# Optimization experiments

Measured on AMD Instinct MI355X. Metric: run time of the kernel, lower is better.

## Reference

```python
import jax, jax.numpy as jnp
import numpy as np
import math

B, S, V, E, H, MD, P, W = 2, 2048, 32000, 512, 1024, 256, 4096, 128

def setup_inputs() -> dict:
    key = jax.random.key(0)
    ks = jax.random.split(key, 24)
    sc = 0.02
    inp = {}
    inp['input_ids'] = jax.random.randint(ks[0], (B, S), 0, V)
    inp['untied_token_ids'] = jax.random.randint(ks[1], (P,), 0, V)
    inp['emb'] = jax.random.normal(ks[2], (V, E), jnp.float32) * sc
    inp['w_ih'] = jax.random.normal(ks[3], (3 * H, E), jnp.float32) * sc
    inp['w_hh'] = jax.random.normal(ks[4], (3 * H, H), jnp.float32) * sc
    inp['b_ih'] = jnp.zeros((3 * H,), jnp.float32)
    inp['b_hh'] = jnp.zeros((3 * H,), jnp.float32)
    inp['wq'] = jax.random.normal(ks[5], (MD, H), jnp.float32) * sc
    inp['bq'] = jnp.zeros((MD,), jnp.float32)
    inp['wk'] = jax.random.normal(ks[6], (MD, H), jnp.float32) * sc
    inp['bk'] = jnp.zeros((MD,), jnp.float32)
    inp['wv'] = jax.random.normal(ks[7], (E, H), jnp.float32) * sc
    inp['bv'] = jnp.zeros((E,), jnp.float32)
    inp['wg'] = jax.random.normal(ks[8], (1, H), jnp.float32) * sc
    inp['bg'] = jnp.zeros((1,), jnp.float32)
    inp['w_fc'] = jax.random.normal(ks[9], (4 * E, H), jnp.float32) * sc
    inp['b_fc'] = jnp.zeros((4 * E,), jnp.float32)
    inp['w_hp'] = jax.random.normal(ks[10], (E, 4 * E), jnp.float32) * sc
    inp['b_hp'] = jnp.zeros((E,), jnp.float32)
    inp['out_bias'] = jnp.zeros((V,), jnp.float32)
    inp['w_ph'] = jax.random.normal(ks[11], (P, E), jnp.float32) * sc
    inp['b_ph'] = jnp.zeros((P,), jnp.float32)
    inp['mem_scale'] = jnp.asarray(6.0, jnp.float32)
    return inp

def _gru(x, w_ih, w_hh, b_ih, b_hh):
    # x: [B,S,E] -> states [B,S,H]. Precompute input gates outside scan.
    gi = jnp.einsum('bse,ge->bsg', x, w_ih) + b_ih  # [B,S,3H]
    h0 = jnp.zeros((x.shape[0], w_hh.shape[1]), x.dtype)
    def step(h, gi_t):
        hg = h @ w_hh.T + b_hh
        gir, giz, gin = jnp.split(gi_t, 3, axis=-1)
        hgr, hgz, hgn = jnp.split(hg, 3, axis=-1)
        r = jax.nn.sigmoid(gir + hgr)
        z = jax.nn.sigmoid(giz + hgz)
        n = jnp.tanh(gin + r * hgn)
        h_new = (1.0 - z) * n + z * h
        return h_new, h_new
    _, hs = jax.lax.scan(step, h0, jnp.swapaxes(gi, 0, 1))  # [S,B,H]
    return jnp.swapaxes(hs, 0, 1)

def _forward(input_ids, untied_token_ids, emb, w_ih, w_hh, b_ih, b_hh, wq, bq,
             wk, bk, wv, bv, wg, bg, w_fc, b_fc, w_hp, b_hp, out_bias, w_ph,
             b_ph, mem_scale):
    x = emb[input_ids]                                   # [B,S,E]
    states = _gru(x, w_ih, w_hh, b_ih, b_hh)             # [B,S,H]
    hf = jnp.square(jax.nn.relu(states @ w_fc.T + b_fc)) # [B,S,4E]
    base_feat = hf @ w_hp.T + b_hp                       # [B,S,E]
    base_logits = base_feat @ emb.T + out_bias           # [B,S,V]
    base_partial = base_feat @ w_ph.T + b_ph             # [B,S,P]
    q = states @ wq.T + bq                               # [B,S,MD]
    k = states @ wk.T + bk
    v = states @ wv.T + bv                               # [B,S,E]
    scores = jnp.einsum('bqd,bkd->bqk', q, k) / math.sqrt(q.shape[-1])
    pos = jnp.arange(input_ids.shape[1])
    mask = (pos[None, :] < pos[:, None]) & (pos[None, :] >= pos[:, None] - W)
    neg = jnp.finfo(scores.dtype).min
    attn = jax.nn.softmax(jnp.where(mask[None], scores, neg), axis=-1)
    attn = attn * mask[None]
    attn = attn / jnp.clip(attn.sum(-1, keepdims=True), 1e-6)
    ctx = jnp.einsum('bqk,bke->bqe', attn, v)            # [B,S,E]
    gate = jax.nn.sigmoid(states @ wg.T + bg)            # [B,S,1]
    total_partial = base_partial + gate * mem_scale * (ctx @ w_ph.T + b_ph)
    return base_logits.at[:, :, untied_token_ids].add(total_partial)

def reference(input_ids, untied_token_ids, emb, w_ih, w_hh, b_ih, b_hh, wq,
              bq, wk, bk, wv, bv, wg, bg, w_fc, b_fc, w_hp, b_hp, out_bias,
              w_ph, b_ph, mem_scale):
    return _forward(input_ids, untied_token_ids, emb, w_ih, w_hh, b_ih, b_hh,
                    wq, bq, wk, bk, wv, bv, wg, bg, w_fc, b_fc, w_hp, b_hp,
                    out_bias, w_ph, b_ph, mem_scale)
```

## Files before the change

### kernel.cpp

```cpp
#include <hip/hip_runtime.h>
#include <math.h>

typedef __attribute__((ext_vector_type(4))) float f32x4;
typedef __attribute__((ext_vector_type(2))) float f32x2;
typedef __attribute__((ext_vector_type(8))) __bf16 bf16x8;
typedef __attribute__((ext_vector_type(4))) __bf16 bf16x4;
typedef __attribute__((ext_vector_type(4))) unsigned int u32x4;

#define DI __device__ __forceinline__

constexpr int Bd = 2, Sd = 2048, Vd = 32000, Ed = 512, Hd = 1024, MDd = 256, Pd = 4096, Wd = 128;
constexpr int BS = Bd * Sd;
constexpr int GBLK = 128;

DI float sigmoidf_(float x) { return 1.0f / (1.0f + expf(-x)); }

template<int EPI>
__global__ __launch_bounds__(256) void gemm_h(
    const __bf16* __restrict__ A, const __bf16* __restrict__ B,
    const float* __restrict__ bias, float* __restrict__ C,
    __bf16* __restrict__ Ch,
    int M, int N, int K, int ldc,
    const float* __restrict__ gate, const float* __restrict__ msp,
    const int* __restrict__ untied)
{
  __shared__ __attribute__((aligned(16))) __bf16 As[128 * 32];
  __shared__ __attribute__((aligned(16))) __bf16 Bs[128 * 32];
  const int tid  = threadIdx.x;
  const int lane = tid & 63, w = tid >> 6;
  const int m0 = blockIdx.y * 128, n0 = blockIdx.x * 128;
  const int wrow = (w >> 1) * 64, wcol = (w & 1) * 64;

  f32x4 acc[4][4] = {};
  const int nk = K >> 5;

  const int srow = (w << 5) + (lane >> 2);
  const int sce  = (lane & 3) << 3;
  __bf16* lA0 = As + (w << 10);
  __bf16* lB0 = Bs + (w << 10);

  for (int kt = 0; kt < nk; ++kt) {
    const int k0 = kt << 5;
    __syncthreads();
    {
      const __bf16* ga0 = A + (size_t)(m0 + srow) * K + k0 + sce;
      const __bf16* ga1 = A + (size_t)(m0 + srow + 16) * K + k0 + sce;
      const __bf16* gb0 = B + (size_t)(n0 + srow) * K + k0 + sce;
      const __bf16* gb1 = B + (size_t)(n0 + srow + 16) * K + k0 + sce;
      __builtin_amdgcn_global_load_lds(
          (const __attribute__((address_space(1))) void*)ga0,
          (__attribute__((address_space(3))) void*)lA0, 16, 0, 0);
      __builtin_amdgcn_global_load_lds(
          (const __attribute__((address_space(1))) void*)ga1,
          (__attribute__((address_space(3))) void*)(lA0 + 512), 16, 0, 0);
      __builtin_amdgcn_global_load_lds(
          (const __attribute__((address_space(1))) void*)gb0,
          (__attribute__((address_space(3))) void*)lB0, 16, 0, 0);
      __builtin_amdgcn_global_load_lds(
          (const __attribute__((address_space(1))) void*)gb1,
          (__attribute__((address_space(3))) void*)(lB0 + 512), 16, 0, 0);
    }
    __syncthreads();

    bf16x8 af[4], bfr[4];
    #pragma unroll
    for (int t2 = 0; t2 < 4; ++t2) {
      const int ra = wrow + t2 * 16 + (lane & 15);
      const int rb = wcol + t2 * 16 + (lane & 15);
      const int cs = (lane >> 4) << 3;
      af[t2]  = *reinterpret_cast<const bf16x8*>(As + ra * 32 + cs);
      bfr[t2] = *reinterpret_cast<const bf16x8*>(Bs + rb * 32 + cs);
    }
    #pragma unroll
    for (int mi = 0; mi < 4; ++mi)
      #pragma unroll
      for (int ni = 0; ni < 4; ++ni)
        acc[mi][ni] = __builtin_amdgcn_mfma_f32_16x16x32_bf16(af[mi], bfr[ni], acc[mi][ni], 0, 0, 0);
  }

  const float ms = (EPI == 3) ? msp[0] : 0.f;
  #pragma unroll
  for (int mi = 0; mi < 4; ++mi) {
    #pragma unroll
    for (int ni = 0; ni < 4; ++ni) {
      const int cc = n0 + wcol + ni * 16 + (lane & 15);
      const float bv = bias ? bias[cc] : 0.f;
      #pragma unroll
      for (int rg = 0; rg < 4; ++rg) {
        const int rr = m0 + wrow + mi * 16 + (lane >> 4) * 4 + rg;
        const float v = acc[mi][ni][rg];
        if (EPI == 0) {
          C[(size_t)rr * ldc + cc] = v + bv;
        } else if (EPI == 1) {
          float u = fmaxf(v + bv, 0.f);
          Ch[(size_t)rr * ldc + cc] = (__bf16)(u * u);
        } else if (EPI == 2) {
          float o = v + bv;
          C[(size_t)rr * ldc + cc] = o;
          Ch[(size_t)rr * ldc + cc] = (__bf16)o;
        } else {
          float g = 1.f + gate[rr] * ms;
          atomicAdd(&C[(size_t)rr * ldc + untied[cc]], v + g * bv);
        }
      }
    }
  }
}

__global__ __launch_bounds__(256) void convh(
    const float* __restrict__ s, __bf16* __restrict__ d, int n)
{
  const int i = (blockIdx.x * 256 + threadIdx.x) * 8;
  if (i >= n) return;
  f32x4 a = *reinterpret_cast<const f32x4*>(s + i);
  f32x4 b = *reinterpret_cast<const f32x4*>(s + i + 4);
  bf16x8 o;
  o[0] = (__bf16)a.x; o[1] = (__bf16)a.y; o[2] = (__bf16)a.z; o[3] = (__bf16)a.w;
  o[4] = (__bf16)b.x; o[5] = (__bf16)b.y; o[6] = (__bf16)b.z; o[7] = (__bf16)b.w;
  *reinterpret_cast<bf16x8*>(d + i) = o;
}

DI void poll2_coherent(const unsigned long long* p, u32x4& a) {
  asm volatile("global_load_dwordx4 %0, %1, off sc0 sc1\n\t"
               "s_waitcnt vmcnt(0)"
               : "=&v"(a) : "v"(p) : "memory");
}

__global__ __launch_bounds__(1024) void gru_kernel(
    const float* __restrict__ gi,
    const float* __restrict__ w_hh,
    const float* __restrict__ b_hh,
    __bf16* __restrict__ statesh,
    unsigned long long* __restrict__ hb)
{
  __shared__ float hsm[Hd];
  __shared__ float gpre_sm[2][48];
  __shared__ float pubst[16];
  const int bid = blockIdx.x, tid = threadIdx.x;
  const int lane = tid & 63, wv = tid >> 6;
  const int b  = bid >> 6;
  const int gb = bid & 63;
  const int j  = gb * 16 + wv;

  f32x4 wr[4], wz[4], wn[4];
  #pragma unroll
  for (int c = 0; c < 4; ++c) {
    const int k = lane * 4 + c * 256;
    wr[c] = *reinterpret_cast<const f32x4*>(w_hh + (size_t)(0 * Hd + j) * Hd + k);
    wz[c] = *reinterpret_cast<const f32x4*>(w_hh + (size_t)(1 * Hd + j) * Hd + k);
    wn[c] = *reinterpret_cast<const f32x4*>(w_hh + (size_t)(2 * Hd + j) * Hd + k);
  }
  const float br = b_hh[j], bz = b_hh[Hd + j], bn = b_hh[2 * Hd + j];

  for (int i = tid; i < Hd; i += 1024) hsm[i] = 0.f;
  if (tid < 48) {
    const int g = tid >> 4, o = tid & 15;
    gpre_sm[0][tid] = gi[(size_t)b * Sd * 3 * Hd + g * Hd + gb * 16 + o];
  }
  __syncthreads();

  const int slot0 = (((tid & 511) + (gb << 3)) & 511) * 2;
  const bool poller = (tid < 512);

  for (int t = 0; t < Sd; ++t) {
    float d0 = 0, d1 = 0, d2 = 0;
    #pragma unroll
    for (int c = 0; c < 4; ++c) {
      f32x4 hv = *reinterpret_cast<const f32x4*>(&hsm[lane * 4 + c * 256]);
      d0 += wr[c].x*hv.x + wr[c].y*hv.y + wr[c].z*hv.z + wr[c].w*hv.w;
      d1 += wz[c].x*hv.x + wz[c].y*hv.y + wz[c].z*hv.z + wz[c].w*hv.w;
      d2 += wn[c].x*hv.x + wn[c].y*hv.y + wn[c].z*hv.z + wn[c].w*hv.w;
    }
    #pragma unroll
    for (int off = 32; off > 0; off >>= 1) {
      d0 += __shfl_xor(d0, off, 64);
      d1 += __shfl_xor(d1, off, 64);
      d2 += __shfl_xor(d2, off, 64);
    }

    const unsigned tagu = (unsigned)(t + 1);
    const unsigned long long tag = (unsigned long long)(t + 1);
    const int par = (t + 1) & 1;
    unsigned long long* hbp = hb + ((size_t)par * 2 + b) * Hd;

    const float pgr = gpre_sm[t & 1][wv];
    const float pgz = gpre_sm[t & 1][16 + wv];
    const float pgn = gpre_sm[t & 1][32 + wv];
    const float a  = (lane == 0) ? (pgr + d0 + br) : (pgz + d1 + bz);
    const float sg = sigmoidf_(a);
    const float r  = __shfl(sg, 0, 64);
    const float z  = __shfl(sg, 1, 64);
    const float n  = tanhf(pgn + r * (d2 + bn));
    const float ho = hsm[j];
    const float h  = (1.f - z) * n + z * ho;
    if (lane == 0) pubst[wv] = h;

    __syncthreads();

    if (tid < 16) {
      const float hv = pubst[tid];
      __hip_atomic_store(&hbp[gb * 16 + tid],
                         (tag << 32) | (unsigned long long)__float_as_uint(hv),
                         __ATOMIC_RELAXED, __HIP_MEMORY_SCOPE_AGENT);
    }

    if (tid >= 512 && tid < 560) {
      const int q = tid - 512;
      const int g = q >> 4, o = q & 15;
      const int tn = (t + 1 < Sd) ? (t + 1) : t;
      gpre_sm[par][q] = gi[((size_t)b * Sd + tn) * 3 * Hd + g * Hd + gb * 16 + o];
    }
    if (tid >= 576 && tid < 592) {
      const int q = tid - 576;
      statesh[((size_t)b * Sd + t) * Hd + gb * 16 + q] = (__bf16)pubst[q];
    }

    if (poller && t + 1 < Sd) {
      float v0 = 0, v1 = 0;
      bool done = false;
      for (int rounds = 0; rounds < 16384 && !done; ++rounds) {
        u32x4 a4;
        poll2_coherent(&hbp[slot0], a4);
        if (a4[1] == tagu && a4[3] == tagu) {
          v0 = __uint_as_float(a4[0]); v1 = __uint_as_float(a4[2]);
          done = true;
        } else if (rounds >= 6) {
          __builtin_amdgcn_s_sleep(1);
        }
      }
      if (!done) {
        bool f0 = false, f1 = false;
        do {
          unsigned long long x0, x1;
          if (!f0) x0 = __hip_atomic_load(&hbp[slot0 + 0], __ATOMIC_RELAXED, __HIP_MEMORY_SCOPE_AGENT);
          if (!f1) x1 = __hip_atomic_load(&hbp[slot0 + 1], __ATOMIC_RELAXED, __HIP_MEMORY_SCOPE_AGENT);
          if (!f0 && (x0 >> 32) == tag) { v0 = __uint_as_float((unsigned)x0); f0 = true; }
          if (!f1 && (x1 >> 32) == tag) { v1 = __uint_as_float((unsigned)x1); f1 = true; }
        } while (!(f0 && f1));
      }
      hsm[slot0]     = v0;
      hsm[slot0 + 1] = v1;
    }
    __syncthreads();
  }
}

__global__ __launch_bounds__(128) void embed_kernel(
    const int* __restrict__ ids, const float* __restrict__ emb, __bf16* __restrict__ xh)
{
  const int row = blockIdx.x;
  const int tok = ids[row];
  f32x4 v = reinterpret_cast<const f32x4*>(emb + (size_t)tok * Ed)[threadIdx.x];
  bf16x4 o;
  o[0] = (__bf16)v.x; o[1] = (__bf16)v.y; o[2] = (__bf16)v.z; o[3] = (__bf16)v.w;
  reinterpret_cast<bf16x4*>(xh + (size_t)row * Ed)[threadIdx.x] = o;
}

__global__ __launch_bounds__(256) void gate_kernel(
    const __bf16* __restrict__ statesh, const float* __restrict__ wg,
    const float* __restrict__ bg, float* __restrict__ gate)
{
  const int row = blockIdx.x * 4 + (threadIdx.x >> 6);
  const int lane = threadIdx.x & 63;
  const __bf16* sp = statesh + (size_t)row * Hd + lane * 16;
  bf16x8 a0 = *reinterpret_cast<const bf16x8*>(sp);
  bf16x8 a1 = *reinterpret_cast<const bf16x8*>(sp + 8);
  float s = 0;
  #pragma unroll
  for (int i = 0; i < 8; ++i)
    s += (float)a0[i] * wg[lane * 16 + i] + (float)a1[i] * wg[lane * 16 + 8 + i];
  #pragma unroll
  for (int off = 32; off > 0; off >>= 1) s += __shfl_down(s, off, 64);
  if (lane == 0) gate[row] = sigmoidf_(s + bg[0]);
}

__global__ __launch_bounds__(256) void attn_kernel(
    const float* __restrict__ qkv, const float* __restrict__ featb,
    __bf16* __restrict__ ffh,
    const float* __restrict__ gate, const float* __restrict__ msp)
{
  const int row = blockIdx.x;
  const int b = row >> 11, qi = row & (Sd - 1);
  const int tid = threadIdx.x, lane = tid & 63, wv = tid >> 6;
  __shared__ float qs[MDd];
  __shared__ float sc[Wd];
  qs[tid] = qkv[(size_t)row * 1024 + tid];
  __syncthreads();
  const int lo = (qi > Wd) ? (qi - Wd) : 0;
  const int len = qi - lo;
  const float gm = gate[row] * msp[0];
  for (int jj = wv; jj < len; jj += 4) {
    const float* kr = qkv + (size_t)(b * Sd + lo + jj) * 1024 + 256;
    f32x4 kv = *reinterpret_cast<const f32x4*>(kr + lane * 4);
    f32x4 qv = *reinterpret_cast<const f32x4*>(&qs[lane * 4]);
    float s = kv.x * qv.x + kv.y * qv.y + kv.z * qv.z + kv.w * qv.w;
    #pragma unroll
    for (int off = 32; off > 0; off >>= 1) s += __shfl_down(s, off, 64);
    if (lane == 0) sc[jj] = s * 0.0625f;
  }
  __syncthreads();
  if (wv == 0 && len > 0) {
    float m = -3.4e38f;
    for (int jj = lane; jj < len; jj += 64) m = fmaxf(m, sc[jj]);
    #pragma unroll
    for (int off = 32; off > 0; off >>= 1) m = fmaxf(m, __shfl_xor(m, off, 64));
    float ssum = 0;
    for (int jj = lane; jj < len; jj += 64) { float e = expf(sc[jj] - m); sc[jj] = e; ssum += e; }
    #pragma unroll
    for (int off = 32; off > 0; off >>= 1) ssum += __shfl_xor(ssum, off, 64);
    const float inv = 1.f / ssum;
    for (int jj = lane; jj < len; jj += 64) sc[jj] *= inv;
  }
  __syncthreads();
  #pragma unroll
  for (int e0 = 0; e0 < Ed; e0 += 256) {
    const int e = e0 + tid;
    float a = 0;
    for (int jj = 0; jj < len; ++jj)
      a += sc[jj] * qkv[(size_t)(b * Sd + lo + jj) * 1024 + 512 + e];
    ffh[(size_t)row * Ed + e] = (__bf16)(featb[(size_t)row * Ed + e] + gm * a);
  }
}

extern "C" void kernel_launch(void* const* d_in, const int* in_sizes, int n_in,
                              void* d_out, int out_size, void* d_ws, size_t ws_size,
                              hipStream_t stream)
{
  const int*   ids    = (const int*)d_in[0];
  const int*   untied = (const int*)d_in[1];
  const float* emb    = (const float*)d_in[2];
  const float* w_ih   = (const float*)d_in[3];
  const float* w_hh   = (const float*)d_in[4];
  const float* b_ih   = (const float*)d_in[5];
  const float* b_hh   = (const float*)d_in[6];
  const float* wq     = (const float*)d_in[7];
  const float* bq     = (const float*)d_in[8];
  const float* wk     = (const float*)d_in[9];
  const float* bk     = (const float*)d_in[10];
  const float* wv     = (const float*)d_in[11];
  const float* bv     = (const float*)d_in[12];
  const float* wg     = (const float*)d_in[13];
  const float* bg     = (const float*)d_in[14];
  const float* w_fc   = (const float*)d_in[15];
  const float* b_fc   = (const float*)d_in[16];
  const float* w_hp   = (const float*)d_in[17];
  const float* b_hp   = (const float*)d_in[18];
  const float* out_b  = (const float*)d_in[19];
  const float* w_ph   = (const float*)d_in[20];
  const float* b_ph   = (const float*)d_in[21];
  const float* msc    = (const float*)d_in[22];
  float* out = (float*)d_out;

  char* W = (char*)d_ws;
  size_t off = 0;
  auto nxt = [&](size_t bytes) { char* p = W + off; off += (bytes + 255) & ~(size_t)255; return p; };
  float*  gi      = (float*) nxt((size_t)BS * 3 * Hd * 4);
  __bf16* statesh = (__bf16*)nxt((size_t)BS * Hd * 2);
  float*  featb   = (float*) nxt((size_t)BS * Ed * 4);
  __bf16* embh    = (__bf16*)nxt((size_t)Vd * Ed * 2);
  __bf16* wih_h   = (__bf16*)nxt((size_t)3 * Hd * Ed * 2);
  __bf16* wfc_h   = (__bf16*)nxt((size_t)4 * Ed * Hd * 2);
  __bf16* whp_h   = (__bf16*)nxt((size_t)Ed * 4 * Ed * 2);
  __bf16* wqkv_h  = (__bf16*)nxt((size_t)1024 * Hd * 2);
  __bf16* wph_h   = (__bf16*)nxt((size_t)Pd * Ed * 2);
  __bf16* xh      = (__bf16*)nxt((size_t)BS * Ed * 2);
  float*  bqkv    = (float*) nxt(1024 * 4);
  unsigned long long* hb = (unsigned long long*)nxt(2 * 2 * Hd * 8);
  float*  gateb   = (float*) nxt((size_t)BS * 4);
  __bf16* hfh    = (__bf16*)gi;
  __bf16* feat_h = (__bf16*)((char*)gi + 16777216);
  __bf16* ffh    = (__bf16*)((char*)gi + 20971520);
  float*  qkv    = (float*) ((char*)gi + 25165824);

  hipMemsetAsync(hb, 0, 2 * 2 * Hd * sizeof(unsigned long long), stream);

  auto cv = [&](const float* s, __bf16* d, size_t n) {
    convh<<<(int)((n / 8 + 255) / 256), 256, 0, stream>>>(s, d, (int)n);
  };
  cv(emb,  embh,  (size_t)Vd * Ed);
  cv(w_ih, wih_h, (size_t)3 * Hd * Ed);
  cv(w_fc, wfc_h, (size_t)4 * Ed * Hd);
  cv(w_hp, whp_h, (size_t)Ed * 4 * Ed);
  cv(wq,   wqkv_h,                 (size_t)MDd * Hd);
  cv(wk,   wqkv_h + (size_t)MDd * Hd,  (size_t)MDd * Hd);
  cv(wv,   wqkv_h + (size_t)512 * Hd,  (size_t)Ed * Hd);
  cv(w_ph, wph_h, (size_t)Pd * Ed);
  hipMemcpyAsync(bqkv,       bq, MDd * 4, hipMemcpyDeviceToDevice, stream);
  hipMemcpyAsync(bqkv + MDd, bk, MDd * 4, hipMemcpyDeviceToDevice, stream);
  hipMemcpyAsync(bqkv + 512, bv, Ed * 4,  hipMemcpyDeviceToDevice, stream);

  embed_kernel<<<BS, 128, 0, stream>>>(ids, emb, xh);
  gemm_h<0><<<dim3(3 * Hd / 128, BS / 128), 256, 0, stream>>>(
      xh, wih_h, b_ih, gi, nullptr, BS, 3 * Hd, Ed, 3 * Hd, nullptr, nullptr, nullptr);
  gru_kernel<<<GBLK, 1024, 0, stream>>>(gi, w_hh, b_hh, statesh, hb);
  gemm_h<1><<<dim3(4 * Ed / 128, BS / 128), 256, 0, stream>>>(
      statesh, wfc_h, b_fc, nullptr, hfh, BS, 4 * Ed, Hd, 4 * Ed, nullptr, nullptr, nullptr);
  gemm_h<2><<<dim3(Ed / 128, BS / 128), 256, 0, stream>>>(
      hfh, whp_h, b_hp, featb, feat_h, BS, Ed, 4 * Ed, Ed, nullptr, nullptr, nullptr);
  gemm_h<0><<<dim3(Vd / 128, BS / 128), 256, 0, stream>>>(
      feat_h, embh, out_b, out, nullptr, BS, Vd, Ed, Vd, nullptr, nullptr, nullptr);
  gemm_h<0><<<dim3(1024 / 128, BS / 128), 256, 0, stream>>>(
      statesh, wqkv_h, bqkv, qkv, nullptr, BS, 1024, Hd, 1024, nullptr, nullptr, nullptr);
  gate_kernel<<<BS / 4, 256, 0, stream>>>(statesh, wg, bg, gateb);
  attn_kernel<<<BS, 256, 0, stream>>>(qkv, featb, ffh, gateb, msc);
  gemm_h<3><<<dim3(Pd / 128, BS / 128), 256, 0, stream>>>(
      ffh, wph_h, b_ph, out, nullptr, BS, Pd, Ed, Vd, gateb, msc, untied);
}
```

Before: 6.400 ms.

## Overlap weight bf16 conversions with GRU recurrence using extra blocks; widen attention

```diff
diff --git a/kernel.cpp b/kernel.cpp
--- a/kernel.cpp
+++ b/kernel.cpp
@@ -12,6 +12,7 @@
 constexpr int Bd = 2, Sd = 2048, Vd = 32000, Ed = 512, Hd = 1024, MDd = 256, Pd = 4096, Wd = 128;
 constexpr int BS = Bd * Sd;
 constexpr int GBLK = 128;
+constexpr int CBLK = 96;
 
 DI float sigmoidf_(float x) { return 1.0f / (1.0f + expf(-x)); }
 
@@ -120,6 +121,19 @@
   *reinterpret_cast<bf16x8*>(d + i) = o;
 }
 
+DI void conv_range(const float* __restrict__ s, __bf16* __restrict__ d,
+                   size_t n, int wb, int tid)
+{
+  for (size_t i = ((size_t)wb * 1024 + tid) * 8; i < n; i += (size_t)CBLK * 1024 * 8) {
+    f32x4 a = *reinterpret_cast<const f32x4*>(s + i);
+    f32x4 b = *reinterpret_cast<const f32x4*>(s + i + 4);
+    bf16x8 o;
+    o[0] = (__bf16)a.x; o[1] = (__bf16)a.y; o[2] = (__bf16)a.z; o[3] = (__bf16)a.w;
+    o[4] = (__bf16)b.x; o[5] = (__bf16)b.y; o[6] = (__bf16)b.z; o[7] = (__bf16)b.w;
+    *reinterpret_cast<bf16x8*>(d + i) = o;
+  }
+}
+
 DI void poll2_coherent(const unsigned long long* p, u32x4& a) {
   asm volatile("global_load_dwordx4 %0, %1, off sc0 sc1\n\t"
                "s_waitcnt vmcnt(0)"
@@ -131,12 +145,31 @@
     const float* __restrict__ w_hh,
     const float* __restrict__ b_hh,
     __bf16* __restrict__ statesh,
-    unsigned long long* __restrict__ hb)
-{
+    unsigned long long* __restrict__ hb,
+    const float* __restrict__ emb,  __bf16* __restrict__ embh,
+    const float* __restrict__ wfc,  __bf16* __restrict__ wfc_h,
+    const float* __restrict__ whp,  __bf16* __restrict__ whp_h,
+    const float* __restrict__ wq,   const float* __restrict__ wk,
+    const float* __restrict__ wvv,  __bf16* __restrict__ wqkv_h,
+    const float* __restrict__ wph,  __bf16* __restrict__ wph_h)
+{
+  const int bid = blockIdx.x, tid = threadIdx.x;
+
+  if (bid >= GBLK) {
+    const int wb = bid - GBLK;
+    conv_range(emb, embh, (size_t)Vd * Ed, wb, tid);
+    conv_range(wfc, wfc_h, (size_t)4 * Ed * Hd, wb, tid);
+    conv_range(whp, whp_h, (size_t)Ed * 4 * Ed, wb, tid);
+    conv_range(wq,  wqkv_h,                      (size_t)MDd * Hd, wb, tid);
+    conv_range(wk,  wqkv_h + (size_t)MDd * Hd,   (size_t)MDd * Hd, wb, tid);
+    conv_range(wvv, wqkv_h + (size_t)512 * Hd,   (size_t)Ed * Hd,  wb, tid);
+    conv_range(wph, wph_h, (size_t)Pd * Ed, wb, tid);
+    return;
+  }
+
   __shared__ float hsm[Hd];
   __shared__ float gpre_sm[2][48];
   __shared__ float pubst[16];
-  const int bid = blockIdx.x, tid = threadIdx.x;
   const int lane = tid & 63, wv = tid >> 6;
   const int b  = bid >> 6;
   const int gb = bid & 63;
@@ -274,7 +307,7 @@
   if (lane == 0) gate[row] = sigmoidf_(s + bg[0]);
 }
 
-__global__ __launch_bounds__(256) void attn_kernel(
+__global__ __launch_bounds__(512) void attn_kernel(
     const float* __restrict__ qkv, const float* __restrict__ featb,
     __bf16* __restrict__ ffh,
     const float* __restrict__ gate, const float* __restrict__ msp)
@@ -284,12 +317,12 @@
   const int tid = threadIdx.x, lane = tid & 63, wv = tid >> 6;
   __shared__ float qs[MDd];
   __shared__ float sc[Wd];
-  qs[tid] = qkv[(size_t)row * 1024 + tid];
+  if (tid < MDd) qs[tid] = qkv[(size_t)row * 1024 + tid];
   __syncthreads();
   const int lo = (qi > Wd) ? (qi - Wd) : 0;
   const int len = qi - lo;
   const float gm = gate[row] * msp[0];
-  for (int jj = wv; jj < len; jj += 4) {
+  for (int jj = wv; jj < len; jj += 8) {
     const float* kr = qkv + (size_t)(b * Sd + lo + jj) * 1024 + 256;
     f32x4 kv = *reinterpret_cast<const f32x4*>(kr + lane * 4);
     f32x4 qv = *reinterpret_cast<const f32x4*>(&qs[lane * 4]);
@@ -312,9 +345,8 @@
     for (int jj = lane; jj < len; jj += 64) sc[jj] *= inv;
   }
   __syncthreads();
-  #pragma unroll
-  for (int e0 = 0; e0 < Ed; e0 += 256) {
-    const int e = e0 + tid;
+  {
+    const int e = tid;
     float a = 0;
     for (int jj = 0; jj < len; ++jj)
       a += sc[jj] * qkv[(size_t)(b * Sd + lo + jj) * 1024 + 512 + e];
@@ -374,17 +406,8 @@
 
   hipMemsetAsync(hb, 0, 2 * 2 * Hd * sizeof(unsigned long long), stream);
 
-  auto cv = [&](const float* s, __bf16* d, size_t n) {
-    convh<<<(int)((n / 8 + 255) / 256), 256, 0, stream>>>(s, d, (int)n);
-  };
-  cv(emb,  embh,  (size_t)Vd * Ed);
-  cv(w_ih, wih_h, (size_t)3 * Hd * Ed);
-  cv(w_fc, wfc_h, (size_t)4 * Ed * Hd);
-  cv(w_hp, whp_h, (size_t)Ed * 4 * Ed);
-  cv(wq,   wqkv_h,                 (size_t)MDd * Hd);
-  cv(wk,   wqkv_h + (size_t)MDd * Hd,  (size_t)MDd * Hd);
-  cv(wv,   wqkv_h + (size_t)512 * Hd,  (size_t)Ed * Hd);
-  cv(w_ph, wph_h, (size_t)Pd * Ed);
+  convh<<<(int)(((size_t)3 * Hd * Ed / 8 + 255) / 256), 256, 0, stream>>>(
+      w_ih, wih_h, 3 * Hd * Ed);
   hipMemcpyAsync(bqkv,       bq, MDd * 4, hipMemcpyDeviceToDevice, stream);
   hipMemcpyAsync(bqkv + MDd, bk, MDd * 4, hipMemcpyDeviceToDevice, stream);
   hipMemcpyAsync(bqkv + 512, bv, Ed * 4,  hipMemcpyDeviceToDevice, stream);
@@ -392,7 +415,9 @@
   embed_kernel<<<BS, 128, 0, stream>>>(ids, emb, xh);
   gemm_h<0><<<dim3(3 * Hd / 128, BS / 128), 256, 0, stream>>>(
       xh, wih_h, b_ih, gi, nullptr, BS, 3 * Hd, Ed, 3 * Hd, nullptr, nullptr, nullptr);
-  gru_kernel<<<GBLK, 1024, 0, stream>>>(gi, w_hh, b_hh, statesh, hb);
+  gru_kernel<<<GBLK + CBLK, 1024, 0, stream>>>(
+      gi, w_hh, b_hh, statesh, hb,
+      emb, embh, w_fc, wfc_h, w_hp, whp_h, wq, wk, wv, wqkv_h, w_ph, wph_h);
   gemm_h<1><<<dim3(4 * Ed / 128, BS / 128), 256, 0, stream>>>(
       statesh, wfc_h, b_fc, nullptr, hfh, BS, 4 * Ed, Hd, 4 * Ed, nullptr, nullptr, nullptr);
   gemm_h<2><<<dim3(Ed / 128, BS / 128), 256, 0, stream>>>(
@@ -402,7 +427,7 @@
   gemm_h<0><<<dim3(1024 / 128, BS / 128), 256, 0, stream>>>(
       statesh, wqkv_h, bqkv, qkv, nullptr, BS, 1024, Hd, 1024, nullptr, nullptr, nullptr);
   gate_kernel<<<BS / 4, 256, 0, stream>>>(statesh, wg, bg, gateb);
-  attn_kernel<<<BS, 256, 0, stream>>>(qkv, featb, ffh, gateb, msc);
+  attn_kernel<<<BS, 512, 0, stream>>>(qkv, featb, ffh, gateb, msc);
   gemm_h<3><<<dim3(Pd / 128, BS / 128), 256, 0, stream>>>(
       ffh, wph_h, b_ph, out, nullptr, BS, Pd, Ed, Vd, gateb, msc, untied);
 }
```

Result: slower. 6.563 ms (+2.6%).
